# Performance work log

Measured on AMD Instinct MI355X. Metric: run time of the kernel, lower is better.

## Reference

```python
import jax, jax.numpy as jnp
import numpy as np

B, T, A, C = 8, 256, 2, 128
R, H, OUT = 128, 128, 256  # readin_dim, session_embed_size, out_count


def _uni(k, shape, fan_in):
    # matches torch kaiming_uniform_(a=sqrt(5)) / nn.Linear default: U(-1/sqrt(fan_in), 1/sqrt(fan_in))
    b = 1.0 / np.sqrt(fan_in)
    return jax.random.uniform(k, shape, jnp.float32, -b, b)


def setup_inputs() -> dict:
    key = jax.random.key(0)
    ks = jax.random.split(key, 16)
    return {
        "state_in": jax.random.normal(ks[0], (B, T, A, C), jnp.float32),
        "session": jax.random.normal(ks[1], (B, H), jnp.float32),
        "subject": jax.random.normal(ks[2], (B, H), jnp.float32),
        "array": jax.random.normal(ks[3], (B, A, H), jnp.float32),
        "query": jax.random.normal(ks[4], (R,), jnp.float32),
        "pos_embeds": _uni(ks[5], (C, R), R),
        # key_project: Linear(R+H, R) -> GELU -> Linear(R, R); weights stored [in, out]
        "kW1": _uni(ks[6], (R + H, R), R + H), "kb1": _uni(ks[7], (R,), R + H),
        "kW2": _uni(ks[8], (R, R), R), "kb2": _uni(ks[9], (R,), R),
        # value_project: Linear(1+R+H, R) -> GELU -> Linear(R, OUT)
        # concat order in forward is [pos_embed (R), session (H), state_in (1)]
        "vW1": _uni(ks[10], (R + H + 1, R), R + H + 1), "vb1": _uni(ks[11], (R,), R + H + 1),
        "vW2": _uni(ks[12], (R, OUT), R), "vb2": _uni(ks[13], (OUT,), R),
    }


def reference(state_in, session, subject, array, query, pos_embeds,
              kW1, kb1, kW2, kb2, vW1, vb1, vW2, vb2):
    r = pos_embeds.shape[-1]
    h = session.shape[-1]
    scale = jnp.sqrt(jnp.asarray(r, state_in.dtype))
    # keys: cat([pos (c,r) expand b, session (b,h) expand c]) -> MLP. Decompose the
    # first Linear over the concat blocks (same math, no expanded concat buffer).
    kh = (pos_embeds @ kW1[:r])[None, :, :] + (session @ kW1[r:])[:, None, :] + kb1  # [b,c,r]
    keys = jax.nn.gelu(kh, approximate=False) @ kW2 + kb2                           # [b,c,r]
    # values: cat([pos, session, state_in]) over (b,t,a,c) -> MLP, decomposed likewise
    vh = ((pos_embeds @ vW1[:r])[None, None, None, :, :]
          + (session @ vW1[r:r + h])[:, None, None, None, :]
          + state_in[..., None] * vW1[r + h]
          + vb1)                                                                     # [b,t,a,c,r]
    values = jax.nn.gelu(vh, approximate=False) @ vW2 + vb2                          # [b,t,a,c,out]
    scores = jnp.einsum('bcr,r->bc', keys, query) / scale
    w = jax.nn.softmax(scores, axis=-1)                                              # [b,c]
    return jnp.einsum('bc,btach->btah', w, values)                                   # [b,t,a,out]
```

## Files before the change

### kernel.cpp

```cpp
#include <hip/hip_runtime.h>
#include <math.h>

#define B_ 8
#define T_ 256
#define A_ 2
#define C_ 128
#define R_ 128
#define H_ 128
#define OUT_ 256

#define WS_PCK 0
#define WS_PCV 16384
#define WS_PSK 32768
#define WS_PSV 33792
#define WS_QK  34816
#define WS_W1  36864
#define WS_W2  167936
#define WS_W3  299008
#define WS_S0  430080
#define WS_TOTAL 431104

__device__ __forceinline__ float gelu_fast(float x) {
    const float ax = fabsf(x);
    float q = fmaf(ax, 0.019527f, 0.000343654f);
    q = fmaf(q, ax, 0.1151945f);
    q = fmaf(q, ax, 0.19685217f);
    q = fmaf(q, ax, 1.0f);
    const float r  = __builtin_amdgcn_rcpf(q);
    const float r2 = r * r;
    const float r4 = r2 * r2;
    return fmaf(-0.5f * ax, r4, fmaxf(x, 0.0f));
}

__global__ __launch_bounds__(256) void prep_kernel(
    const float* __restrict__ session,
    const float* __restrict__ query,
    const float* __restrict__ pos,
    const float* __restrict__ kW1,
    const float* __restrict__ kb1,
    const float* __restrict__ kW2,
    const float* __restrict__ vW1,
    const float* __restrict__ vb1,
    float* __restrict__ ws)
{
    const int g = blockIdx.x * 256 + threadIdx.x;
    if (g < 16384) {
        const int c = g >> 7, r = g & 127;
        float acc = 0.0f;
        #pragma unroll 16
        for (int k = 0; k < R_; ++k)
            acc += pos[c * R_ + k] * kW1[k * R_ + r];
        ws[WS_PCK + g] = acc;
    } else if (g < 32768) {
        const int e = g - 16384;
        const int c = e >> 7, r = e & 127;
        float acc = 0.0f;
        #pragma unroll 16
        for (int k = 0; k < R_; ++k)
            acc += pos[c * R_ + k] * vW1[k * R_ + r];
        ws[WS_PCV + e] = acc;
    } else if (g < 33792) {
        const int e = g - 32768;
        const int b = e >> 7, r = e & 127;
        float acc = kb1[r];
        #pragma unroll 16
        for (int k = 0; k < H_; ++k)
            acc += session[b * H_ + k] * kW1[(R_ + k) * R_ + r];
        ws[WS_PSK + e] = acc;
    } else if (g < 34816) {
        const int e = g - 33792;
        const int b = e >> 7, r = e & 127;
        float acc = vb1[r];
        #pragma unroll 16
        for (int k = 0; k < H_; ++k)
            acc += session[b * H_ + k] * vW1[(R_ + k) * R_ + r];
        ws[WS_PSV + e] = acc;
    } else if (g < 34944) {
        const int r = g - 34816;
        float acc = 0.0f;
        #pragma unroll 16
        for (int j = 0; j < R_; ++j)
            acc += kW2[r * R_ + j] * query[j];
        ws[WS_QK + r] = acc;
    }
}

__global__ __launch_bounds__(1024) void softmax_coef_kernel(
    const float* __restrict__ vW1,
    float* __restrict__ ws)
{
    __shared__ float pskL[R_];
    __shared__ float qkL[R_];
    __shared__ float part8[8][C_];
    __shared__ float sc[C_];
    __shared__ float red[C_];
    __shared__ float wL[C_];

    const int b   = blockIdx.x;
    const int tid = threadIdx.x;
    const int q   = tid >> 7;
    const int c   = tid & 127;

    if (tid < 128) {
        pskL[tid] = ws[WS_PSK + b * R_ + tid];
        qkL[tid]  = ws[WS_QK + tid];
    }
    __syncthreads();

    const float* __restrict__ pckc = ws + WS_PCK + c * R_ + q * 16;
    float acc = 0.0f;
    #pragma unroll
    for (int i = 0; i < 16; ++i) {
        const float x = pckc[i] + pskL[q * 16 + i];
        acc += gelu_fast(x) * qkL[q * 16 + i];
    }
    part8[q][c] = acc;
    __syncthreads();

    if (tid < 128) {
        float s = part8[0][tid];
        #pragma unroll
        for (int j = 1; j < 8; ++j) s += part8[j][tid];
        s *= 0.08838834764831845f;
        sc[tid]  = s;
        red[tid] = s;
    }
    __syncthreads();
    for (int st = 64; st > 0; st >>= 1) {
        if (tid < st) red[tid] = fmaxf(red[tid], red[tid + st]);
        __syncthreads();
    }
    const float m = red[0];
    __syncthreads();
    if (tid < 128) {
        const float e = __expf(sc[tid] - m);
        sc[tid]  = e;
        red[tid] = e;
    }
    __syncthreads();
    for (int st = 64; st > 0; st >>= 1) {
        if (tid < st) red[tid] += red[tid + st];
        __syncthreads();
    }
    if (tid < 128) wL[tid] = sc[tid] / red[0];
    __syncthreads();

    const int r  = c;
    const int cq = q;
    const float vr  = vW1[(R_ + H_) * R_ + r];
    const float vr2 = vr * vr;
    const float vr3 = vr2 * vr;
    const float psv_r = ws[WS_PSV + b * R_ + r];

    float s0acc = 0.0f;
    #pragma unroll 4
    for (int i = 0; i < 16; ++i) {
        const int c2 = cq * 16 + i;
        const float cc  = ws[WS_PCV + c2 * R_ + r] + psv_r;
        const float wgt = wL[c2];
        const float ax = fabsf(cc);
        float qq = fmaf(ax, 0.019527f, 0.000343654f);
        qq = fmaf(qq, ax, 0.1151945f);
        qq = fmaf(qq, ax, 0.19685217f);
        qq = fmaf(qq, ax, 1.0f);
        const float qi  = __builtin_amdgcn_rcpf(qq);
        const float qi2 = qi * qi;
        const float h   = 0.5f * qi2 * qi2;
        const float Phi = (cc >= 0.0f) ? (1.0f - h) : h;
        const float cc2 = cc * cc;
        const float phi = 0.3989422804f * __expf(-0.5f * cc2);
        const float g0 = cc * Phi;
        const float g1 = fmaf(cc, phi, Phi);
        const float g2 = 0.5f * phi * (2.0f - cc2);
        const float g3 = phi * cc * (cc2 - 4.0f) * (1.0f / 6.0f);
        const size_t idx = (size_t)(b * C_ + c2) * R_ + r;
        ws[WS_W1 + idx] = wgt * g1 * vr;
        ws[WS_W2 + idx] = wgt * g2 * vr2;
        ws[WS_W3 + idx] = wgt * g3 * vr3;
        s0acc += wgt * g0;
    }
    part8[cq][r] = s0acc;
    __syncthreads();
    if (tid < 128) {
        float s = part8[0][tid];
        #pragma unroll
        for (int j = 1; j < 8; ++j) s += part8[j][tid];
        ws[WS_S0 + b * R_ + tid] = s;
    }
}

__global__ __launch_bounds__(256) void main_kernel(
    const float* __restrict__ state,
    const float* __restrict__ vW2,
    const float* __restrict__ vb2,
    const float* __restrict__ ws,
    float* __restrict__ out)
{
    __shared__ __align__(16) float sv[8 * C_];
    __shared__ float4 smem[2][8][R_];
    __shared__ float4 p4lo[R_];
    __shared__ float4 p4hi[R_];

    const int blk = blockIdx.x;
    const int b   = blk >> 6;
    const int grp = blk & 63;
    const int tid = threadIdx.x;
    const int k   = tid & 31;
    const int seg = tid >> 5;
    const int r0  = k * 4;

    const float* __restrict__ srow = state + (size_t)(b * 512 + grp * 8) * C_;
    #pragma unroll
    for (int i = 0; i < 4; ++i) sv[tid + 256 * i] = srow[tid + 256 * i];
    __syncthreads();

    const size_t pbase = (size_t)(b * C_) * R_ + r0;
    const float* __restrict__ W1p = ws + WS_W1 + pbase;
    const float* __restrict__ W2p = ws + WS_W2 + pbase;
    const float* __restrict__ W3p = ws + WS_W3 + pbase;

    float4 a[8];
    #pragma unroll
    for (int j = 0; j < 8; ++j) a[j] = make_float4(0.f, 0.f, 0.f, 0.f);

    const int cbeg = seg * 16;
    #pragma unroll 2
    for (int i = 0; i < 16; ++i) {
        const int c = cbeg + i;
        const float4 w1 = *(const float4*)(W1p + (size_t)c * R_);
        const float4 w2 = *(const float4*)(W2p + (size_t)c * R_);
        const float4 w3 = *(const float4*)(W3p + (size_t)c * R_);
        #pragma unroll
        for (int j = 0; j < 8; ++j) {
            const float s  = sv[j * C_ + c];
            const float s2 = s * s;
            const float s3 = s2 * s;
            a[j].x = fmaf(w1.x, s, a[j].x); a[j].x = fmaf(w2.x, s2, a[j].x); a[j].x = fmaf(w3.x, s3, a[j].x);
            a[j].y = fmaf(w1.y, s, a[j].y); a[j].y = fmaf(w2.y, s2, a[j].y); a[j].y = fmaf(w3.y, s3, a[j].y);
            a[j].z = fmaf(w1.z, s, a[j].z); a[j].z = fmaf(w2.z, s2, a[j].z); a[j].z = fmaf(w3.z, s3, a[j].z);
            a[j].w = fmaf(w1.w, s, a[j].w); a[j].w = fmaf(w2.w, s2, a[j].w); a[j].w = fmaf(w3.w, s3, a[j].w);
        }
    }

    smem[0][seg][r0 + 0] = make_float4(a[0].x, a[1].x, a[2].x, a[3].x);
    smem[0][seg][r0 + 1] = make_float4(a[0].y, a[1].y, a[2].y, a[3].y);
    smem[0][seg][r0 + 2] = make_float4(a[0].z, a[1].z, a[2].z, a[3].z);
    smem[0][seg][r0 + 3] = make_float4(a[0].w, a[1].w, a[2].w, a[3].w);
    smem[1][seg][r0 + 0] = make_float4(a[4].x, a[5].x, a[6].x, a[7].x);
    smem[1][seg][r0 + 1] = make_float4(a[4].y, a[5].y, a[6].y, a[7].y);
    smem[1][seg][r0 + 2] = make_float4(a[4].z, a[5].z, a[6].z, a[7].z);
    smem[1][seg][r0 + 3] = make_float4(a[4].w, a[5].w, a[6].w, a[7].w);
    __syncthreads();

    if (tid < 128) {
        float4 lo = smem[0][0][tid];
        float4 hi = smem[1][0][tid];
        #pragma unroll
        for (int sg = 1; sg < 8; ++sg) {
            const float4 tl = smem[0][sg][tid];
            const float4 th = smem[1][sg][tid];
            lo.x += tl.x; lo.y += tl.y; lo.z += tl.z; lo.w += tl.w;
            hi.x += th.x; hi.y += th.y; hi.z += th.z; hi.w += th.w;
        }
        const float s0v = ws[WS_S0 + b * R_ + tid];
        lo.x += s0v; lo.y += s0v; lo.z += s0v; lo.w += s0v;
        hi.x += s0v; hi.y += s0v; hi.z += s0v; hi.w += s0v;
        p4lo[tid] = lo;
        p4hi[tid] = hi;
    }
    __syncthreads();

    float4 (*ep)[8][64] = (float4 (*)[8][64])smem;
    const int hq = tid & 63;
    const int kq = tid >> 6;
    const int h0 = hq * 4;

    float4 o[8];
    #pragma unroll
    for (int j = 0; j < 8; ++j) o[j] = make_float4(0.f, 0.f, 0.f, 0.f);
    const int rrb = kq * 32;
    #pragma unroll 4
    for (int i = 0; i < 32; ++i) {
        const int rr = rrb + i;
        const float4 plo = p4lo[rr];
        const float4 phi = p4hi[rr];
        const float4 wv4 = *(const float4*)(vW2 + rr * OUT_ + h0);
        o[0].x = fmaf(plo.x, wv4.x, o[0].x); o[0].y = fmaf(plo.x, wv4.y, o[0].y);
        o[0].z = fmaf(plo.x, wv4.z, o[0].z); o[0].w = fmaf(plo.x, wv4.w, o[0].w);
        o[1].x = fmaf(plo.y, wv4.x, o[1].x); o[1].y = fmaf(plo.y, wv4.y, o[1].y);
        o[1].z = fmaf(plo.y, wv4.z, o[1].z); o[1].w = fmaf(plo.y, wv4.w, o[1].w);
        o[2].x = fmaf(plo.z, wv4.x, o[2].x); o[2].y = fmaf(plo.z, wv4.y, o[2].y);
        o[2].z = fmaf(plo.z, wv4.z, o[2].z); o[2].w = fmaf(plo.z, wv4.w, o[2].w);
        o[3].x = fmaf(plo.w, wv4.x, o[3].x); o[3].y = fmaf(plo.w, wv4.y, o[3].y);
        o[3].z = fmaf(plo.w, wv4.z, o[3].z); o[3].w = fmaf(plo.w, wv4.w, o[3].w);
        o[4].x = fmaf(phi.x, wv4.x, o[4].x); o[4].y = fmaf(phi.x, wv4.y, o[4].y);
        o[4].z = fmaf(phi.x, wv4.z, o[4].z); o[4].w = fmaf(phi.x, wv4.w, o[4].w);
        o[5].x = fmaf(phi.y, wv4.x, o[5].x); o[5].y = fmaf(phi.y, wv4.y, o[5].y);
        o[5].z = fmaf(phi.y, wv4.z, o[5].z); o[5].w = fmaf(phi.y, wv4.w, o[5].w);
        o[6].x = fmaf(phi.z, wv4.x, o[6].x); o[6].y = fmaf(phi.z, wv4.y, o[6].y);
        o[6].z = fmaf(phi.z, wv4.z, o[6].z); o[6].w = fmaf(phi.z, wv4.w, o[6].w);
        o[7].x = fmaf(phi.w, wv4.x, o[7].x); o[7].y = fmaf(phi.w, wv4.y, o[7].y);
        o[7].z = fmaf(phi.w, wv4.z, o[7].z); o[7].w = fmaf(phi.w, wv4.w, o[7].w);
    }
    #pragma unroll
    for (int j = 0; j < 8; ++j) ep[kq][j][hq] = o[j];
    __syncthreads();

    const int row  = tid >> 5;
    const int hqa  = tid & 31;
    float* __restrict__ orow = out + (size_t)(b * 512 + grp * 8) * OUT_ + row * OUT_;
    #pragma unroll
    for (int half = 0; half < 2; ++half) {
        const int hh = hqa + half * 32;
        const float4 e0 = ep[0][row][hh];
        const float4 e1 = ep[1][row][hh];
        const float4 e2 = ep[2][row][hh];
        const float4 e3 = ep[3][row][hh];
        const float4 bias = *(const float4*)(vb2 + hh * 4);
        float4 oo;
        oo.x = e0.x + e1.x + e2.x + e3.x + bias.x;
        oo.y = e0.y + e1.y + e2.y + e3.y + bias.y;
        oo.z = e0.z + e1.z + e2.z + e3.z + bias.z;
        oo.w = e0.w + e1.w + e2.w + e3.w + bias.w;
        *(float4*)(orow + hh * 4) = oo;
    }
}

extern "C" void kernel_launch(void* const* d_in, const int* in_sizes, int n_in,
                              void* d_out, int out_size, void* d_ws, size_t ws_size,
                              hipStream_t stream) {
    const float* state   = (const float*)d_in[0];
    const float* session = (const float*)d_in[1];
    const float* query   = (const float*)d_in[4];
    const float* pos     = (const float*)d_in[5];
    const float* kW1     = (const float*)d_in[6];
    const float* kb1     = (const float*)d_in[7];
    const float* kW2     = (const float*)d_in[8];
    const float* vW1     = (const float*)d_in[10];
    const float* vb1     = (const float*)d_in[11];
    const float* vW2     = (const float*)d_in[12];
    const float* vb2     = (const float*)d_in[13];

    float* ws  = (float*)d_ws;
    float* out = (float*)d_out;

    prep_kernel<<<137, 256, 0, stream>>>(session, query, pos, kW1, kb1, kW2,
                                         vW1, vb1, ws);
    softmax_coef_kernel<<<B_, 1024, 0, stream>>>(vW1, ws);
    main_kernel<<<B_ * 64, 256, 0, stream>>>(state, vW2, vb2, ws, out);
}
```

Before: 110.8 us.

## Split softmax and coefficient computation into separate kernels for wider parallelism

```diff
diff --git a/kernel.cpp b/kernel.cpp
--- a/kernel.cpp
+++ b/kernel.cpp
@@ -14,6 +14,7 @@
 #define WS_PSK 32768
 #define WS_PSV 33792
 #define WS_QK  34816
+#define WS_WSM 34944
 #define WS_W1  36864
 #define WS_W2  167936
 #define WS_W3  299008
@@ -82,19 +83,18 @@
         for (int j = 0; j < R_; ++j)
             acc += kW2[r * R_ + j] * query[j];
         ws[WS_QK + r] = acc;
-    }
-}
-
-__global__ __launch_bounds__(1024) void softmax_coef_kernel(
-    const float* __restrict__ vW1,
-    float* __restrict__ ws)
+    } else if (g < 35968) {
+        ws[WS_S0 + (g - 34944)] = 0.0f;
+    }
+}
+
+__global__ __launch_bounds__(1024) void softmax_kernel(float* __restrict__ ws)
 {
     __shared__ float pskL[R_];
     __shared__ float qkL[R_];
     __shared__ float part8[8][C_];
     __shared__ float sc[C_];
     __shared__ float red[C_];
-    __shared__ float wL[C_];
 
     const int b   = blockIdx.x;
     const int tid = threadIdx.x;
@@ -142,51 +142,47 @@
         if (tid < st) red[tid] += red[tid + st];
         __syncthreads();
     }
-    if (tid < 128) wL[tid] = sc[tid] / red[0];
-    __syncthreads();
-
-    const int r  = c;
-    const int cq = q;
+    if (tid < 128) ws[WS_WSM + b * C_ + tid] = sc[tid] / red[0];
+}
+
+__global__ __launch_bounds__(256) void coef_kernel(
+    const float* __restrict__ vW1,
+    float* __restrict__ ws)
+{
+    const int blk = blockIdx.x;
+    const int b   = blk >> 6;
+    const int cp  = blk & 63;
+    const int tid = threadIdx.x;
+    const int c   = cp * 2 + (tid >> 7);
+    const int r   = tid & 127;
+
     const float vr  = vW1[(R_ + H_) * R_ + r];
     const float vr2 = vr * vr;
     const float vr3 = vr2 * vr;
-    const float psv_r = ws[WS_PSV + b * R_ + r];
-
-    float s0acc = 0.0f;
-    #pragma unroll 4
-    for (int i = 0; i < 16; ++i) {
-        const int c2 = cq * 16 + i;
-        const float cc  = ws[WS_PCV + c2 * R_ + r] + psv_r;
-        const float wgt = wL[c2];
-        const float ax = fabsf(cc);
-        float qq = fmaf(ax, 0.019527f, 0.000343654f);
-        qq = fmaf(qq, ax, 0.1151945f);
-        qq = fmaf(qq, ax, 0.19685217f);
-        qq = fmaf(qq, ax, 1.0f);
-        const float qi  = __builtin_amdgcn_rcpf(qq);
-        const float qi2 = qi * qi;
-        const float h   = 0.5f * qi2 * qi2;
-        const float Phi = (cc >= 0.0f) ? (1.0f - h) : h;
-        const float cc2 = cc * cc;
-        const float phi = 0.3989422804f * __expf(-0.5f * cc2);
-        const float g0 = cc * Phi;
-        const float g1 = fmaf(cc, phi, Phi);
-        const float g2 = 0.5f * phi * (2.0f - cc2);
-        const float g3 = phi * cc * (cc2 - 4.0f) * (1.0f / 6.0f);
-        const size_t idx = (size_t)(b * C_ + c2) * R_ + r;
-        ws[WS_W1 + idx] = wgt * g1 * vr;
-        ws[WS_W2 + idx] = wgt * g2 * vr2;
-        ws[WS_W3 + idx] = wgt * g3 * vr3;
-        s0acc += wgt * g0;
-    }
-    part8[cq][r] = s0acc;
-    __syncthreads();
-    if (tid < 128) {
-        float s = part8[0][tid];
-        #pragma unroll
-        for (int j = 1; j < 8; ++j) s += part8[j][tid];
-        ws[WS_S0 + b * R_ + tid] = s;
-    }
+    const float cc  = ws[WS_PCV + c * R_ + r] + ws[WS_PSV + b * R_ + r];
+    const float wgt = ws[WS_WSM + b * C_ + c];
+
+    const float ax = fabsf(cc);
+    float qq = fmaf(ax, 0.019527f, 0.000343654f);
+    qq = fmaf(qq, ax, 0.1151945f);
+    qq = fmaf(qq, ax, 0.19685217f);
+    qq = fmaf(qq, ax, 1.0f);
+    const float qi  = __builtin_amdgcn_rcpf(qq);
+    const float qi2 = qi * qi;
+    const float h   = 0.5f * qi2 * qi2;
+    const float Phi = (cc >= 0.0f) ? (1.0f - h) : h;
+    const float cc2 = cc * cc;
+    const float phi = 0.3989422804f * __expf(-0.5f * cc2);
+    const float g0 = cc * Phi;
+    const float g1 = fmaf(cc, phi, Phi);
+    const float g2 = 0.5f * phi * (2.0f - cc2);
+    const float g3 = phi * cc * (cc2 - 4.0f) * (1.0f / 6.0f);
+
+    const size_t idx = (size_t)(b * C_ + c) * R_ + r;
+    ws[WS_W1 + idx] = wgt * g1 * vr;
+    ws[WS_W2 + idx] = wgt * g2 * vr2;
+    ws[WS_W3 + idx] = wgt * g3 * vr3;
+    atomicAdd(ws + WS_S0 + b * R_ + r, wgt * g0);
 }
 
 __global__ __launch_bounds__(256) void main_kernel(
@@ -344,8 +340,9 @@
     float* ws  = (float*)d_ws;
     float* out = (float*)d_out;
 
-    prep_kernel<<<137, 256, 0, stream>>>(session, query, pos, kW1, kb1, kW2,
+    prep_kernel<<<141, 256, 0, stream>>>(session, query, pos, kW1, kb1, kW2,
                                          vW1, vb1, ws);
-    softmax_coef_kernel<<<B_, 1024, 0, stream>>>(vW1, ws);
+    softmax_kernel<<<B_, 1024, 0, stream>>>(ws);
+    coef_kernel<<<512, 256, 0, stream>>>(vW1, ws);
     main_kernel<<<B_ * 64, 256, 0, stream>>>(state, vW2, vb2, ws, out);
 }
```

Measured after the change: 107.4 us. 1.03x faster.
